# Kernel optimization log

Measured on AMD Instinct MI355X. Metric: run time of the kernel, lower is better.

Reference implementation:

```python
import jax, jax.numpy as jnp
import numpy as np

BN_EPS = 1e-5

def setup_inputs() -> dict:
    key = jax.random.key(0)
    k0, k1, k2, k3, k4 = jax.random.split(key, 5)
    B, N, D, E = 8, 256, 128, 4096
    x_l = jax.random.normal(k0, (B, N, D), dtype=jnp.float32)
    src = jax.random.randint(k1, (E,), 0, N)
    dst = jax.random.randint(k2, (E,), 0, N)
    edge_index_l = jnp.stack([src, dst], axis=0)  # [2, E]
    mask_l = jax.random.randint(k3, (B, N), 0, 2).astype(bool)
    W = jax.random.normal(k4, (D, D), dtype=jnp.float32) * (1.0 / np.sqrt(D))
    b = jnp.zeros((D,), jnp.float32)
    gamma = jnp.ones((D,), jnp.float32)
    beta = jnp.zeros((D,), jnp.float32)
    return {"x_l": x_l, "edge_index_l": edge_index_l, "mask_l": mask_l,
            "W": W, "b": b, "gamma": gamma, "beta": beta}


def reference(x_l, edge_index_l, mask_l, W, b, gamma, beta):
    # x_l: [B, N, D]; edge_index_l: [2, E]; mask_l: [B, N] bool
    B, N, D = x_l.shape
    src, dst = edge_index_l[0], edge_index_l[1]
    # Vectorized replacement of the Python edge loop: edges with dst - src == 3
    # zero the mask at both endpoints (the explicit interaction zeroing in the
    # original is subsumed by the mask, since masked entries never survive).
    cov = (dst - src) == 3  # [E] bool
    hit = jnp.zeros((N,), bool)
    hit = hit.at[src].max(cov)
    hit = hit.at[dst].max(cov)
    mask = mask_l & ~hit[None, :]  # [B, N]
    # Pairwise mask: outer AND minus diagonal
    eye = jnp.eye(N, dtype=bool)
    pair_mask = (mask[:, :, None] & mask[:, None, :]) & ~eye[None]  # [B, N, N]
    # Outer-product interaction: [B, N, N, D]
    interaction = x_l[:, :, None, :] * x_l[:, None, :, :]
    # Linear
    h = jnp.einsum('bijd,ed->bije', interaction, W) + b
    # BatchNorm1d over the masked (selected) rows, training-mode batch stats.
    m = pair_mask[..., None].astype(h.dtype)  # [B, N, N, 1]
    cnt = jnp.maximum(jnp.sum(m), 1.0)
    mean = jnp.sum(h * m, axis=(0, 1, 2)) / cnt  # [D]
    var = jnp.sum(m * (h - mean) ** 2, axis=(0, 1, 2)) / cnt  # biased, as torch BN
    hn = (h - mean) * jax.lax.rsqrt(var + BN_EPS) * gamma + beta
    # Dropout is identity in eval mode; LeakyReLU slope 0.01 (torch default).
    out = jax.nn.leaky_relu(hn, negative_slope=0.01) * m  # zero non-selected entries
    return out, pair_mask
```

## Files before the change

kernel.cpp:

```cpp
#include <hip/hip_runtime.h>

#define B_ 8
#define N_ 256
#define D_ 128
#define E_ 4096

typedef __attribute__((ext_vector_type(8))) short bf16x8;
typedef __attribute__((ext_vector_type(4))) float f32x4;
typedef __attribute__((ext_vector_type(2))) float f32x2;

__device__ inline unsigned int pack2bf(float lo, float hi) {
    unsigned ul = __float_as_uint(lo);
    ul = ul + 0x7FFFu + ((ul >> 16) & 1u);
    unsigned uh = __float_as_uint(hi);
    uh = uh + 0x7FFFu + ((uh >> 16) & 1u);
    return (ul >> 16) | (uh & 0xFFFF0000u);
}

__device__ inline unsigned short f2bf(float f) {
    unsigned u = __float_as_uint(f);
    u = u + 0x7FFFu + ((u >> 16) & 1u);
    return (unsigned short)(u >> 16);
}


__global__ __launch_bounds__(256) void k_prep(const void* __restrict__ edges_raw,
                                              const void* __restrict__ mask_raw,
                                              const float* __restrict__ W,
                                              int* __restrict__ mask,
                                              int* __restrict__ jlist,
                                              int* __restrict__ jcnt,
                                              unsigned short* __restrict__ Wb,
                                              float* __restrict__ Wt,
                                              float* __restrict__ tq,
                                              float* __restrict__ dq) {
    int blk = blockIdx.x, tid = threadIdx.x;
    if (blk >= B_) {
        int idx = (blk - B_) * 256 + tid;
        if (idx < 16384) {
            float w = W[idx];
            Wb[idx] = f2bf(w);
            int e = idx >> 7, d = idx & 127;
            Wt[d * D_ + e] = w;
        } else if (idx < 16512) tq[idx - 16384] = 0.0f;
        else dq[idx - 16512] = 0.0f;
        return;
    }
    int b = blk;
    __shared__ unsigned char hit[N_];
    __shared__ int flags[2];
    __shared__ int wcnt[4], wbase[4];
    hit[tid] = 0;
    if (tid < 2) flags[tid] = 0;
    __syncthreads();

    const unsigned char* mb = (const unsigned char*)mask_raw;
    int loc_m = 0;
    for (int idx = tid; idx < B_ * N_; idx += 256)
        if ((idx & 3) && mb[idx]) loc_m = 1;
    if (loc_m) flags[0] = 1;
    const int* e32 = (const int*)edges_raw;
    int loc_e = 0;
    for (int idx = tid; idx < 2 * E_; idx += 256)
        if ((idx & 1) && e32[idx]) loc_e = 1;
    if (loc_e) flags[1] = 1;
    __syncthreads();

    int mask_is_u8 = flags[0], e_is_i32 = flags[1];
    const long long* e64 = (const long long*)edges_raw;
    for (int e = tid; e < E_; e += 256) {
        int s, d;
        if (e_is_i32) { s = e32[e]; d = e32[E_ + e]; }
        else          { s = (int)e64[e]; d = (int)e64[E_ + e]; }
        if (d - s == 3) { hit[s] = 1; hit[d] = 1; }
    }
    __syncthreads();

    const int* m32 = (const int*)mask_raw;
    int lane = tid & 63, wid = tid >> 6;
    int raw = mask_is_u8 ? (int)(mb[b * N_ + tid] != 0) : (int)(m32[b * N_ + tid] != 0);
    int m = raw && (hit[tid] == 0);
    mask[b * N_ + tid] = m;
    unsigned long long bal = __ballot(m);
    if (lane == 0) wcnt[wid] = __popcll(bal);
    __syncthreads();
    if (tid == 0) {
        int base = 0;
        for (int w = 0; w < 4; ++w) { wbase[w] = base; base += wcnt[w]; }
        jcnt[b] = base;
    }
    __syncthreads();
    if (m) {
        int pos = wbase[wid] + __popcll(bal & ((1ull << lane) - 1ull));
        jlist[b * N_ + pos] = tid;
    }
}

__global__ __launch_bounds__(128) void k_gram3(const float* __restrict__ x,
                                               const int* __restrict__ jlist,
                                               const int* __restrict__ jcnt,
                                               float* __restrict__ part,
                                               float* __restrict__ s1,
                                               float* __restrict__ cdiag) {
    int d = blockIdx.x, b = blockIdx.y, dp = threadIdx.x;
    int kc = jcnt[b];
    const int* jl = jlist + b * N_;
    const float* xb = x + (size_t)b * N_ * D_;
    float c0 = 0, c1 = 0, q0 = 0, q1 = 0, s0 = 0, s1a = 0;
    int t = 0;
    for (; t + 1 < kc; t += 2) {
        int i0 = jl[t], i1 = jl[t + 1];
        float xd0 = xb[i0 * D_ + d], xp0 = xb[i0 * D_ + dp];
        float xd1 = xb[i1 * D_ + d], xp1 = xb[i1 * D_ + dp];
        c0 += xd0 * xp0; q0 += (xd0 * xd0) * (xp0 * xp0); s0 += xd0;
        c1 += xd1 * xp1; q1 += (xd1 * xd1) * (xp1 * xp1); s1a += xd1;
    }
    if (t < kc) {
        int i0 = jl[t];
        float xd0 = xb[i0 * D_ + d], xp0 = xb[i0 * D_ + dp];
        c0 += xd0 * xp0; q0 += (xd0 * xd0) * (xp0 * xp0); s0 += xd0;
    }
    float c = c0 + c1, q = q0 + q1, sa = s0 + s1a;
    part[((size_t)b * D_ + d) * D_ + dp] = c * c - q;
    if (dp == d) cdiag[b * D_ + d] = c;
    if (dp == 0) s1[b * D_ + d] = sa;
}

__global__ __launch_bounds__(128) void k_mw2(const float* __restrict__ part,
                                             const float* __restrict__ Wt,
                                             const float* __restrict__ s1,
                                             const float* __restrict__ cdiag,
                                             float* __restrict__ tq,
                                             float* __restrict__ dq) {
    __shared__ float Ms[D_];
    __shared__ float svs;
    int d = blockIdx.x, e = threadIdx.x;
    float m = 0.0f;
#pragma unroll
    for (int b = 0; b < B_; ++b) m += part[((size_t)b * D_ + d) * D_ + e];
    Ms[e] = m;
    if (e == 0) {
        float sv = 0.0f;
#pragma unroll
        for (int b = 0; b < B_; ++b) {
            float s = s1[b * D_ + d];
            sv += s * s - cdiag[b * D_ + d];
        }
        svs = sv;
    }
    __syncthreads();
    float y = 0.0f;
#pragma unroll 8
    for (int p = 0; p < D_; ++p) y += Ms[p] * Wt[p * D_ + e];
    float wed = Wt[d * D_ + e];
    atomicAdd(tq + e, wed * y);
    atomicAdd(dq + e, wed * svs);
}

__global__ __launch_bounds__(256, 4) void k_mega(const float* __restrict__ x,
                                                 const int* __restrict__ mask,
                                                 const int* __restrict__ jcnt,
                                                 const unsigned short* __restrict__ Wb,
                                                 const float* __restrict__ tq,
                                                 const float* __restrict__ dq,
                                                 const float* __restrict__ bvec,
                                                 const float* __restrict__ gamma,
                                                 const float* __restrict__ beta,
                                                 float* __restrict__ out,
                                                 float* __restrict__ pair) {
    __shared__ int msk[N_];
    __shared__ __align__(16) unsigned char Vsb[32 * 256];
    __shared__ float scs[D_], shs[D_];

    int blk = blockIdx.x, tid = threadIdx.x;
    int b = blk >> 8, i = blk & 255;
    int mi = mask[b * N_ + i];
    f32x4 z4 = (f32x4)(0.f);
    f32x4* outrow = (f32x4*)(out + (size_t)(b * N_ + i) * N_ * D_);

    if (!mi) {
        __builtin_nontemporal_store(0.0f, &pair[(size_t)(b * N_ + i) * N_ + tid]);
#pragma unroll
        for (int p = 0; p < 32; ++p)
            __builtin_nontemporal_store(z4, &outrow[tid + 256 * p]);
        return;
    }

    msk[tid] = mask[b * N_ + tid];

    if (tid < D_) {
        float cnt = 0.0f;
#pragma unroll
        for (int bb = 0; bb < B_; ++bb) {
            float k = (float)jcnt[bb];
            cnt += k * k - k;
        }
        if (cnt < 1.0f) cnt = 1.0f;
        float be = bvec[tid];
        float mean = dq[tid] / cnt + be;
        float eh2 = tq[tid] / cnt + 2.0f * be * mean - be * be;
        float var = eh2 - mean * mean;
        if (var < 0.0f) var = 0.0f;
        float s = gamma[tid] * rsqrtf(var + 1e-5f);
        scs[tid] = s;
        shs[tid] = be * s + beta[tid] - mean * s;
    }
    __syncthreads();

    float pm = (msk[tid] && tid != i) ? 1.0f : 0.0f;
    __builtin_nontemporal_store(pm, &pair[(size_t)(b * N_ + i) * N_ + tid]);

    int w = tid >> 6, l = tid & 63;
    int lo16 = l & 15, hi4 = l >> 4;
    int E0 = w * 32;

    bf16x8 bfrag[2][4];
#pragma unroll
    for (int et = 0; et < 2; ++et) {
        int e = E0 + 2 * lo16 + et;
#pragma unroll
        for (int ks = 0; ks < 4; ++ks)
            bfrag[et][ks] = *(const bf16x8*)(Wb + (size_t)e * D_ + ks * 32 + hi4 * 8);
    }

    float sc0 = scs[E0 + 2 * lo16], sh0 = shs[E0 + 2 * lo16];
    float sc1 = scs[E0 + 2 * lo16 + 1], sh1 = shs[E0 + 2 * lo16 + 1];

    const float* xi = x + (size_t)(b * N_ + i) * D_;
    int d0 = (tid & 7) * 16;
    float4 bx0 = *(const float4*)(xi + d0);
    float4 bx1 = *(const float4*)(xi + d0 + 4);
    float4 bx2 = *(const float4*)(xi + d0 + 8);
    float4 bx3 = *(const float4*)(xi + d0 + 12);

    const float* xb = x + (size_t)b * N_ * D_;
    float* outbase = out + (size_t)(b * N_ + i) * N_ * D_;

    for (int jt = 0; jt < N_; jt += 32) {
        __syncthreads();

        {
            int r = tid >> 3;
            const float* xj = xb + (size_t)(jt + r) * D_;
            int rx = (r & 7) << 4;
            float4 a0 = *(const float4*)(xj + d0);
            float4 a1 = *(const float4*)(xj + d0 + 4);
            float4 a2 = *(const float4*)(xj + d0 + 8);
            float4 a3 = *(const float4*)(xj + d0 + 12);
            uint4 pk1, pk2;
            pk1.x = pack2bf(a0.x * bx0.x, a0.y * bx0.y);
            pk1.y = pack2bf(a0.z * bx0.z, a0.w * bx0.w);
            pk1.z = pack2bf(a1.x * bx1.x, a1.y * bx1.y);
            pk1.w = pack2bf(a1.z * bx1.z, a1.w * bx1.w);
            pk2.x = pack2bf(a2.x * bx2.x, a2.y * bx2.y);
            pk2.y = pack2bf(a2.z * bx2.z, a2.w * bx2.w);
            pk2.z = pack2bf(a3.x * bx3.x, a3.y * bx3.y);
            pk2.w = pack2bf(a3.z * bx3.z, a3.w * bx3.w);
            *(uint4*)(Vsb + r * 256 + ((2 * d0) ^ rx)) = pk1;
            *(uint4*)(Vsb + r * 256 + ((2 * (d0 + 8)) ^ rx)) = pk2;
        }
        __syncthreads();

#pragma unroll
        for (int jq = 0; jq < 2; ++jq) {
            f32x4 acc0 = (f32x4)(0.f);
            f32x4 acc1 = (f32x4)(0.f);
            int rA = jq * 16 + lo16;
            int rbase = rA * 256;
            int rx = (rA & 7) << 4;
#pragma unroll
            for (int ks = 0; ks < 4; ++ks) {
                bf16x8 afr = *(const bf16x8*)(Vsb + rbase + ((ks * 64 + hi4 * 16) ^ rx));
                acc0 = __builtin_amdgcn_mfma_f32_16x16x32_bf16(afr, bfrag[0][ks], acc0, 0, 0, 0);
                acc1 = __builtin_amdgcn_mfma_f32_16x16x32_bf16(afr, bfrag[1][ks], acc1, 0, 0, 0);
            }
#pragma unroll
            for (int v = 0; v < 4; ++v) {
                int j = jt + jq * 16 + hi4 * 4 + v;
                float pmj = (msk[j] && j != i) ? 1.0f : 0.0f;
                float h0 = acc0[v] * sc0 + sh0;
                float h1 = acc1[v] * sc1 + sh1;
                f32x2 o;
                o.x = (h0 >= 0.f ? h0 : 0.01f * h0) * pmj;
                o.y = (h1 >= 0.f ? h1 : 0.01f * h1) * pmj;
                __builtin_nontemporal_store(o,
                    (f32x2*)(outbase + (size_t)j * D_ + E0 + 2 * lo16));
            }
        }
    }
}

extern "C" void kernel_launch(void* const* d_in, const int* in_sizes, int n_in,
                              void* d_out, int out_size, void* d_ws, size_t ws_size,
                              hipStream_t stream) {
    const float* x = (const float*)d_in[0];
    const void* edges = d_in[1];
    const void* mask_in = d_in[2];
    const float* W = (const float*)d_in[3];
    const float* bvec = (const float*)d_in[4];
    const float* gamma = (const float*)d_in[5];
    const float* beta = (const float*)d_in[6];

    float* out = (float*)d_out;
    float* pair = out + (size_t)B_ * N_ * N_ * D_;

    char* ws = (char*)d_ws;
    int* mask = (int*)(ws + 0);
    int* jlist = (int*)(ws + 8192);
    int* jcnt = (int*)(ws + 16384);
    float* tq = (float*)(ws + 16448);
    float* dq = (float*)(ws + 16960);
    unsigned short* Wb = (unsigned short*)(ws + 17472);
    float* Wt = (float*)(ws + 50240);
    float* s1 = (float*)(ws + 115776);
    float* cdiag = (float*)(ws + 119872);
    float* part = (float*)(ws + 123968);

    k_prep<<<73, 256, 0, stream>>>(edges, mask_in, W, mask, jlist, jcnt, Wb, Wt, tq, dq);
    {
        dim3 g(D_, B_);
        k_gram3<<<g, 128, 0, stream>>>(x, jlist, jcnt, part, s1, cdiag);
    }
    k_mw2<<<128, 128, 0, stream>>>(part, Wt, s1, cdiag, tq, dq);
    k_mega<<<B_ * N_, 256, 0, stream>>>(x, mask, jcnt, Wb, tq, dq,
                                        bvec, gamma, beta, out, pair);
}
```

Before: 98.77 us.

## Make k_mega warps independent with per-warp LDS tiles and 16-byte stores

```diff
diff --git a/kernel.cpp b/kernel.cpp
--- a/kernel.cpp
+++ b/kernel.cpp
@@ -7,7 +7,6 @@
 
 typedef __attribute__((ext_vector_type(8))) short bf16x8;
 typedef __attribute__((ext_vector_type(4))) float f32x4;
-typedef __attribute__((ext_vector_type(2))) float f32x2;
 
 __device__ inline unsigned int pack2bf(float lo, float hi) {
     unsigned ul = __float_as_uint(lo);
@@ -157,7 +156,7 @@
     atomicAdd(dq + e, wed * svs);
 }
 
-__global__ __launch_bounds__(256, 4) void k_mega(const float* __restrict__ x,
+__global__ __launch_bounds__(256, 3) void k_mega(const float* __restrict__ x,
                                                  const int* __restrict__ mask,
                                                  const int* __restrict__ jcnt,
                                                  const unsigned short* __restrict__ Wb,
@@ -168,124 +167,115 @@
                                                  const float* __restrict__ beta,
                                                  float* __restrict__ out,
                                                  float* __restrict__ pair) {
-    __shared__ int msk[N_];
-    __shared__ __align__(16) unsigned char Vsb[32 * 256];
-    __shared__ float scs[D_], shs[D_];
+    __shared__ __align__(16) unsigned char Vsb[4][4096];
 
     int blk = blockIdx.x, tid = threadIdx.x;
     int b = blk >> 8, i = blk & 255;
+    int w = tid >> 6, l = tid & 63;
+    int lo16 = l & 15, hi4 = l >> 4;
     int mi = mask[b * N_ + i];
+
+    float* outbase = out + (size_t)(b * N_ + i) * N_ * D_;
     f32x4 z4 = (f32x4)(0.f);
-    f32x4* outrow = (f32x4*)(out + (size_t)(b * N_ + i) * N_ * D_);
 
     if (!mi) {
-        __builtin_nontemporal_store(0.0f, &pair[(size_t)(b * N_ + i) * N_ + tid]);
+        if (w == 0)
+            __builtin_nontemporal_store(z4, (f32x4*)(pair + (size_t)(b * N_ + i) * N_ + 4 * l));
+        f32x4* orow = (f32x4*)outbase;
 #pragma unroll
         for (int p = 0; p < 32; ++p)
-            __builtin_nontemporal_store(z4, &outrow[tid + 256 * p]);
+            __builtin_nontemporal_store(z4, &orow[w * 2048 + l + 64 * p]);
         return;
     }
 
-    msk[tid] = mask[b * N_ + tid];
-
-    if (tid < D_) {
-        float cnt = 0.0f;
-#pragma unroll
-        for (int bb = 0; bb < B_; ++bb) {
-            float k = (float)jcnt[bb];
-            cnt += k * k - k;
-        }
-        if (cnt < 1.0f) cnt = 1.0f;
-        float be = bvec[tid];
-        float mean = dq[tid] / cnt + be;
-        float eh2 = tq[tid] / cnt + 2.0f * be * mean - be * be;
+    int eh = w & 1, rh = w >> 1;
+    int ebase = eh * 64 + 4 * lo16;
+    const int* mrow = mask + b * N_;
+
+    float cnt = 0.0f;
+#pragma unroll
+    for (int bb = 0; bb < B_; ++bb) { float k = (float)jcnt[bb]; cnt += k * k - k; }
+    if (cnt < 1.0f) cnt = 1.0f;
+    float sc[4], sh[4];
+#pragma unroll
+    for (int et = 0; et < 4; ++et) {
+        int e = ebase + et;
+        float be = bvec[e];
+        float mean = dq[e] / cnt + be;
+        float eh2 = tq[e] / cnt + 2.0f * be * mean - be * be;
         float var = eh2 - mean * mean;
         if (var < 0.0f) var = 0.0f;
-        float s = gamma[tid] * rsqrtf(var + 1e-5f);
-        scs[tid] = s;
-        shs[tid] = be * s + beta[tid] - mean * s;
-    }
-    __syncthreads();
-
-    float pm = (msk[tid] && tid != i) ? 1.0f : 0.0f;
-    __builtin_nontemporal_store(pm, &pair[(size_t)(b * N_ + i) * N_ + tid]);
-
-    int w = tid >> 6, l = tid & 63;
-    int lo16 = l & 15, hi4 = l >> 4;
-    int E0 = w * 32;
-
-    bf16x8 bfrag[2][4];
-#pragma unroll
-    for (int et = 0; et < 2; ++et) {
-        int e = E0 + 2 * lo16 + et;
+        float s = gamma[e] * rsqrtf(var + 1e-5f);
+        sc[et] = s;
+        sh[et] = be * s + beta[e] - mean * s;
+    }
+
+    bf16x8 bfrag[4][4];
+#pragma unroll
+    for (int et = 0; et < 4; ++et) {
+        const unsigned short* wrow = Wb + (size_t)(ebase + et) * D_;
 #pragma unroll
         for (int ks = 0; ks < 4; ++ks)
-            bfrag[et][ks] = *(const bf16x8*)(Wb + (size_t)e * D_ + ks * 32 + hi4 * 8);
-    }
-
-    float sc0 = scs[E0 + 2 * lo16], sh0 = shs[E0 + 2 * lo16];
-    float sc1 = scs[E0 + 2 * lo16 + 1], sh1 = shs[E0 + 2 * lo16 + 1];
-
-    const float* xi = x + (size_t)(b * N_ + i) * D_;
-    int d0 = (tid & 7) * 16;
-    float4 bx0 = *(const float4*)(xi + d0);
-    float4 bx1 = *(const float4*)(xi + d0 + 4);
-    float4 bx2 = *(const float4*)(xi + d0 + 8);
-    float4 bx3 = *(const float4*)(xi + d0 + 12);
-
+            bfrag[et][ks] = *(const bf16x8*)(wrow + ks * 32 + hi4 * 8);
+    }
+
+    if (w == 0) {
+        f32x4 pmv;
+#pragma unroll
+        for (int c = 0; c < 4; ++c) {
+            int j = 4 * l + c;
+            pmv[c] = (mrow[j] && j != i) ? 1.0f : 0.0f;
+        }
+        __builtin_nontemporal_store(pmv, (f32x4*)(pair + (size_t)(b * N_ + i) * N_ + 4 * l));
+    }
+
+    const float* xi = x + (size_t)(b * N_ + i) * D_ + hi4 * 32;
+    float4 xa[8];
+#pragma unroll
+    for (int q = 0; q < 8; ++q) xa[q] = *(const float4*)(xi + q * 4);
+
+    unsigned char* Vw = &Vsb[w][0];
     const float* xb = x + (size_t)b * N_ * D_;
-    float* outbase = out + (size_t)(b * N_ + i) * N_ * D_;
-
-    for (int jt = 0; jt < N_; jt += 32) {
-        __syncthreads();
-
-        {
-            int r = tid >> 3;
-            const float* xj = xb + (size_t)(jt + r) * D_;
-            int rx = (r & 7) << 4;
-            float4 a0 = *(const float4*)(xj + d0);
-            float4 a1 = *(const float4*)(xj + d0 + 4);
-            float4 a2 = *(const float4*)(xj + d0 + 8);
-            float4 a3 = *(const float4*)(xj + d0 + 12);
-            uint4 pk1, pk2;
-            pk1.x = pack2bf(a0.x * bx0.x, a0.y * bx0.y);
-            pk1.y = pack2bf(a0.z * bx0.z, a0.w * bx0.w);
-            pk1.z = pack2bf(a1.x * bx1.x, a1.y * bx1.y);
-            pk1.w = pack2bf(a1.z * bx1.z, a1.w * bx1.w);
-            pk2.x = pack2bf(a2.x * bx2.x, a2.y * bx2.y);
-            pk2.y = pack2bf(a2.z * bx2.z, a2.w * bx2.w);
-            pk2.z = pack2bf(a3.x * bx3.x, a3.y * bx3.y);
-            pk2.w = pack2bf(a3.z * bx3.z, a3.w * bx3.w);
-            *(uint4*)(Vsb + r * 256 + ((2 * d0) ^ rx)) = pk1;
-            *(uint4*)(Vsb + r * 256 + ((2 * (d0 + 8)) ^ rx)) = pk2;
-        }
-        __syncthreads();
-
-#pragma unroll
-        for (int jq = 0; jq < 2; ++jq) {
-            f32x4 acc0 = (f32x4)(0.f);
-            f32x4 acc1 = (f32x4)(0.f);
-            int rA = jq * 16 + lo16;
-            int rbase = rA * 256;
-            int rx = (rA & 7) << 4;
-#pragma unroll
-            for (int ks = 0; ks < 4; ++ks) {
-                bf16x8 afr = *(const bf16x8*)(Vsb + rbase + ((ks * 64 + hi4 * 16) ^ rx));
-                acc0 = __builtin_amdgcn_mfma_f32_16x16x32_bf16(afr, bfrag[0][ks], acc0, 0, 0, 0);
-                acc1 = __builtin_amdgcn_mfma_f32_16x16x32_bf16(afr, bfrag[1][ks], acc1, 0, 0, 0);
+    int swz = (lo16 & 7) << 4;
+
+    for (int t = 0; t < 8; ++t) {
+        int j0 = rh * 128 + t * 16;
+
+        const float* xj = xb + (size_t)(j0 + lo16) * D_ + hi4 * 32;
+#pragma unroll
+        for (int q = 0; q < 4; ++q) {
+            float4 a0 = *(const float4*)(xj + q * 8);
+            float4 a1 = *(const float4*)(xj + q * 8 + 4);
+            uint4 pk;
+            pk.x = pack2bf(a0.x * xa[2 * q].x, a0.y * xa[2 * q].y);
+            pk.y = pack2bf(a0.z * xa[2 * q].z, a0.w * xa[2 * q].w);
+            pk.z = pack2bf(a1.x * xa[2 * q + 1].x, a1.y * xa[2 * q + 1].y);
+            pk.w = pack2bf(a1.z * xa[2 * q + 1].z, a1.w * xa[2 * q + 1].w);
+            *(uint4*)(Vw + lo16 * 256 + ((hi4 * 64 + q * 16) ^ swz)) = pk;
+        }
+
+        f32x4 acc[4];
+#pragma unroll
+        for (int et = 0; et < 4; ++et) acc[et] = z4;
+#pragma unroll
+        for (int ks = 0; ks < 4; ++ks) {
+            bf16x8 afr = *(const bf16x8*)(Vw + lo16 * 256 + ((ks * 64 + hi4 * 16) ^ swz));
+#pragma unroll
+            for (int et = 0; et < 4; ++et)
+                acc[et] = __builtin_amdgcn_mfma_f32_16x16x32_bf16(afr, bfrag[et][ks], acc[et], 0, 0, 0);
+        }
+
+#pragma unroll
+        for (int v = 0; v < 4; ++v) {
+            int j = j0 + hi4 * 4 + v;
+            float pmj = (mrow[j] && j != i) ? 1.0f : 0.0f;
+            f32x4 o;
+#pragma unroll
+            for (int et = 0; et < 4; ++et) {
+                float h = acc[et][v] * sc[et] + sh[et];
+                o[et] = (h >= 0.0f ? h : 0.01f * h) * pmj;
             }
-#pragma unroll
-            for (int v = 0; v < 4; ++v) {
-                int j = jt + jq * 16 + hi4 * 4 + v;
-                float pmj = (msk[j] && j != i) ? 1.0f : 0.0f;
-                float h0 = acc0[v] * sc0 + sh0;
-                float h1 = acc1[v] * sc1 + sh1;
-                f32x2 o;
-                o.x = (h0 >= 0.f ? h0 : 0.01f * h0) * pmj;
-                o.y = (h1 >= 0.f ? h1 : 0.01f * h1) * pmj;
-                __builtin_nontemporal_store(o,
-                    (f32x2*)(outbase + (size_t)j * D_ + E0 + 2 * lo16));
-            }
+            __builtin_nontemporal_store(o, (f32x4*)(outbase + (size_t)j * D_ + ebase));
         }
     }
 }
```

Result: slower. 106.2 us (+7.6%).
